# Optimization experiments

Hardware: AMD Instinct MI355X
Metric: run time of the kernel (lower is better)

The kernel has to match this reference:

```python
import jax, jax.numpy as jnp
import numpy as np

B, T, N, K, HD = 4, 32, 1024, 16, 128
IN_CH = 4


def _knn_idx(q, r, k):
    # q, r: [..., 3, N]. dist(n, m) = ||q[..., n] - r[..., m]||
    # expanded-norm form avoids materializing [..., 3, N, N]
    q2 = jnp.sum(q * q, axis=-2)                     # [..., N]
    r2 = jnp.sum(r * r, axis=-2)                     # [..., N]
    qr = jnp.einsum('...cn,...cm->...nm', q, r)      # [..., N, N]
    d2 = q2[..., :, None] + r2[..., None, :] - 2.0 * qr
    _, idx = jax.lax.top_k(-d2, k)                   # smallest-k (sqrt is monotone)
    return idx                                       # [..., N, K]


def _gather_nbrs(feat, idx):
    # feat [B, C, N], idx [B, N, K] -> [B, C, N, K]; out[b,c,n,k] = feat[b,c,idx[b,n,k]]
    return jax.vmap(lambda f, i: f[:, i])(feat, idx)


def _lstm_layer(cur_in, position, pos_past, group_ind, w, b, hd):
    # cur_in [B,T,C,N]; position/pos_past [B,T,4,N]; group_ind [B,T,N,K]
    Bb, Tt, C, Nn = cur_in.shape
    h0 = jnp.zeros((Bb, hd, Nn), cur_in.dtype)
    c0 = jnp.zeros_like(h0)

    def step(carry, inp):
        h, c = carry                                  # [B,hd,N]
        xt, pp, idx = inp                             # [B,C,N], [B,4,N], [B,N,K]
        h_with_pos = jnp.concatenate([pp, h], axis=1) # [B,4+hd,N]
        hg = _gather_nbrs(h_with_pos, idx)            # [B,4+hd,N,K]
        cg = _gather_nbrs(c, idx)                     # [B,hd,N,K]
        # cell subtracts center position from first 4 channels of hidden
        hg = jnp.concatenate([hg[:, :4] - xt[:, :4, :, None], hg[:, 4:]], axis=1)
        xk = jnp.broadcast_to(xt[..., None], xt.shape + (idx.shape[-1],))
        comb = jnp.concatenate([xk, hg], axis=1)      # [B, C+4+hd, N, K]
        gates = jnp.einsum('bink,oi->bonk', comb, w) + b[None, :, None, None]
        ci, cf, co, cgt = jnp.split(gates, 4, axis=1)
        c_next = jax.nn.sigmoid(cf) * cg + jax.nn.sigmoid(ci) * jnp.tanh(cgt)
        h_next = jax.nn.sigmoid(co) * jnp.tanh(c_next)
        h_new = jnp.max(h_next, axis=-1)              # AdaptiveMaxPool2d((None,1)) over K
        c_new = jnp.max(c_next, axis=-1)
        return (h_new, c_new), h_new

    xs = (jnp.moveaxis(cur_in, 1, 0), jnp.moveaxis(pos_past, 1, 0),
          jnp.moveaxis(group_ind, 1, 0))
    (h, c), hs = jax.lax.scan(step, (h0, c0), xs)
    hs = jnp.moveaxis(hs, 0, 1)                       # [B,T,hd,N]
    layer_out = jnp.concatenate([position, hs], axis=2)  # [B,T,4+hd,N]
    return layer_out, h, c


def _forward(x, w0, b0, w1, b1):
    position = x[:, :, :4]                            # [B,T,4,N]
    p3 = position[:, :, :3]
    idx0 = _knn_idx(p3[:, 0], p3[:, 0], K)[:, None]   # [B,1,N,K] (frame 0 vs itself)
    idxr = _knn_idx(p3[:, 1:], p3[:, :-1], K)         # [B,T-1,N,K] (frame t vs t-1)
    group_ind = jnp.concatenate([idx0, idxr], axis=1)  # [B,T,N,K]
    # past-frame positions (t=0 uses frame 0)
    pos_past = jnp.concatenate([position[:, :1], position[:, :-1]], axis=1)
    out0, h, c = _lstm_layer(x,    position, pos_past, group_ind, w0, b0, HD)
    out1, h, c = _lstm_layer(out0, position, pos_past, group_ind, w1, b1, HD)
    return out1, h, c, group_ind


def setup_inputs() -> dict:
    key = jax.random.key(0)
    ks = jax.random.split(key, 3)
    x = jax.random.normal(ks[0], (B, T, IN_CH, N), jnp.float32)
    # 1x1 conv weights flattened to [out, in]; layer0 in=4+4+128=136, layer1 in=132+4+128=264
    w0 = jax.random.normal(ks[1], (4 * HD, IN_CH + 4 + HD), jnp.float32) * 0.05
    b0 = jnp.zeros((4 * HD,), jnp.float32)
    w1 = jax.random.normal(ks[2], (4 * HD, (HD + 4) + 4 + HD), jnp.float32) * 0.05
    b1 = jnp.zeros((4 * HD,), jnp.float32)
    return {"x": x, "w0": w0, "b0": b0, "w1": w1, "b1": b1}


def reference(x, w0, b0, w1, b1):
    out1, h, c, group_ind = _forward(x, w0, b0, w1, b1)
    # match torch shapes: trailing singleton dim
    return out1[..., None], h[..., None], c[..., None], group_ind
```

## Files before the change

### kernel.cpp

```cpp
#include <hip/hip_runtime.h>
#include <math.h>

#define BB 4
#define TT 32
#define NN 1024
#define KK 16
#define HDIM 128
#define NO 512
#define KG 132

#define OUT1_SZ ((size_t)BB*TT*132*NN)
#define OH (OUT1_SZ)
#define OC (OH + (size_t)BB*HDIM*NN)
#define OG (OC + (size_t)BB*HDIM*NN)

__global__ __launch_bounds__(256) void prep_weights(
    const float* __restrict__ w0, const float* __restrict__ w1,
    float* __restrict__ WaT0, float* __restrict__ WgT0,
    float* __restrict__ WaT1, float* __restrict__ WgT1)
{
  int idx = blockIdx.x * 256 + threadIdx.x;
  if (idx >= KG * NO) return;
  int k = idx / NO, o = idx - k * NO;
  WgT0[idx] = w0[o * 136 + 4 + k];
  WgT1[idx] = w1[o * 264 + 132 + k];
  float a1 = w1[o * 264 + k];
  if (k < 4) a1 -= w1[o * 264 + 132 + k];
  WaT1[idx] = a1;
  if (k < 4) WaT0[k * NO + o] = w0[o * 136 + k] - w0[o * 136 + 4 + k];
}

__global__ __launch_bounds__(512) void knn_kernel(
    const float* __restrict__ x, int* __restrict__ gind, float* __restrict__ gfloat)
{
  __shared__ float rx[NN], ry[NN], rz[NN], rr[NN];
  int b = blockIdx.z, t = blockIdx.y;
  int tp = (t == 0) ? 0 : t - 1;
  const float* xr = x + (size_t)(b * TT + tp) * 4 * NN;
  for (int m = threadIdx.x; m < NN; m += 512) {
    float a = xr[m], e = xr[NN + m], c = xr[2 * NN + m];
    rx[m] = a; ry[m] = e; rz[m] = c;
    rr[m] = __fadd_rn(__fadd_rn(__fmul_rn(a, a), __fmul_rn(e, e)), __fmul_rn(c, c));
  }
  __syncthreads();
  int n = blockIdx.x * 512 + threadIdx.x;
  const float* xq = x + (size_t)(b * TT + t) * 4 * NN;
  float qx = xq[n], qy = xq[NN + n], qz = xq[2 * NN + n];
  float q2 = __fadd_rn(__fadd_rn(__fmul_rn(qx, qx), __fmul_rn(qy, qy)), __fmul_rn(qz, qz));
  float bd[KK]; int bi[KK];
#pragma unroll
  for (int i = 0; i < KK; ++i) { bd[i] = 3.402823466e38f; bi[i] = 0; }
  for (int m = 0; m < NN; ++m) {
    float s = __fmaf_rn(qz, rz[m], __fmaf_rn(qy, ry[m], __fmaf_rn(qx, rx[m], 0.0f)));
    float d2 = __fsub_rn(__fadd_rn(q2, rr[m]), __fmul_rn(2.0f, s));
    if (d2 < bd[KK - 1]) {
#pragma unroll
      for (int i = KK - 1; i > 0; --i) {
        float pv = bd[i - 1]; int pi = bi[i - 1];
        if (pv > d2)            { bd[i] = pv; bi[i] = pi; }
        else if (bd[i] > d2)    { bd[i] = d2; bi[i] = m; }
      }
      if (bd[0] > d2) { bd[0] = d2; bi[0] = m; }
    }
  }
  size_t base = ((size_t)(b * TT + t) * NN + n) * KK;
#pragma unroll
  for (int i = 0; i < KK; ++i) { gind[base + i] = bi[i]; gfloat[base + i] = (float)bi[i]; }
}

template<int KA>
__global__ __launch_bounds__(256) void gemm_ag(
    const float* __restrict__ WgT, const float* __restrict__ WaT,
    const float* __restrict__ bias,
    const float* __restrict__ x,
    const float* __restrict__ h_g, const float* __restrict__ h_a,
    int t, int tp,
    float* __restrict__ Aout, float* __restrict__ Gout)
{
  __shared__ float sXg[44][68];
  __shared__ float sWg[44][64];
  __shared__ float sXa[(KA == 4) ? 4 : 44][68];
  __shared__ float sWa[(KA == 4) ? 4 : 44][64];

  int tid = threadIdx.x;
  int nb = blockIdx.x * 64, ob = blockIdx.y * 64, b = blockIdx.z;
  int ty = tid >> 4, tx = tid & 15;
  int o0 = ty * 4, n0 = tx * 4;

  float accG[4][4] = {};
  float accA[4][4];
#pragma unroll
  for (int i = 0; i < 4; ++i) {
    float bv = bias[ob + o0 + i];
#pragma unroll
    for (int j = 0; j < 4; ++j) accA[i][j] = bv;
  }

  const float* xp_prev = x + (size_t)(b * TT + tp) * 4 * NN;
  const float* xp_cur  = x + (size_t)(b * TT + t) * 4 * NN;

#pragma unroll
  for (int ic = 0; ic < 3; ++ic) {
    const int kc0 = ic * 44;
    for (int i2 = tid; i2 < 44 * 64; i2 += 256) {
      int k = i2 >> 6, o = i2 & 63;
      sWg[k][o] = WgT[(size_t)(kc0 + k) * NO + ob + o];
      if (KA == 132) sWa[k][o] = WaT[(size_t)(kc0 + k) * NO + ob + o];
    }
    if (KA == 4 && ic == 0 && tid < 4 * 64) {
      int k = tid >> 6, o = tid & 63;
      sWa[k][o] = WaT[k * NO + ob + o];
    }
    if (ic == 0) {
      int k = tid >> 6, n = tid & 63;
      sXg[k][n] = xp_prev[k * NN + nb + n];
      sXa[k][n] = xp_cur[k * NN + nb + n];
    }
    {
      const int j0 = (ic == 0) ? 0 : (kc0 - 4);
      const int jc = (ic == 0) ? 40 : 44;
      for (int i2 = tid; i2 < 64 * jc; i2 += 256) {
        int n = i2 / jc, jj = i2 - n * jc;
        int krow = j0 + jj + 4 - kc0;
        sXg[krow][n] = h_g[((size_t)b * NN + nb + n) * HDIM + j0 + jj];
        if (KA == 132)
          sXa[krow][n] = h_a[((size_t)b * NN + nb + n) * HDIM + j0 + jj];
      }
    }
    __syncthreads();

    if (KA == 4 && ic == 0) {
#pragma unroll
      for (int k = 0; k < 4; ++k) {
        float4 wa = *(const float4*)&sWa[k][o0];
        float4 xa = *(const float4*)&sXa[k][n0];
        float wv[4] = {wa.x, wa.y, wa.z, wa.w};
        float xv[4] = {xa.x, xa.y, xa.z, xa.w};
#pragma unroll
        for (int i = 0; i < 4; ++i)
#pragma unroll
          for (int j = 0; j < 4; ++j) accA[i][j] = fmaf(wv[i], xv[j], accA[i][j]);
      }
    }
#pragma unroll 4
    for (int k = 0; k < 44; ++k) {
      float4 wg = *(const float4*)&sWg[k][o0];
      float4 xg = *(const float4*)&sXg[k][n0];
      float wv[4] = {wg.x, wg.y, wg.z, wg.w};
      float xv[4] = {xg.x, xg.y, xg.z, xg.w};
#pragma unroll
      for (int i = 0; i < 4; ++i)
#pragma unroll
        for (int j = 0; j < 4; ++j) accG[i][j] = fmaf(wv[i], xv[j], accG[i][j]);
      if (KA == 132) {
        float4 wa = *(const float4*)&sWa[k][o0];
        float4 xa = *(const float4*)&sXa[k][n0];
        float wv2[4] = {wa.x, wa.y, wa.z, wa.w};
        float xv2[4] = {xa.x, xa.y, xa.z, xa.w};
#pragma unroll
        for (int i = 0; i < 4; ++i)
#pragma unroll
          for (int j = 0; j < 4; ++j) accA[i][j] = fmaf(wv2[i], xv2[j], accA[i][j]);
      }
    }
    __syncthreads();
  }
#pragma unroll
  for (int j = 0; j < 4; ++j) {
    size_t row = ((size_t)b * NN + nb + n0 + j) * NO + ob + o0;
    *(float4*)&Gout[row] = make_float4(accG[0][j], accG[1][j], accG[2][j], accG[3][j]);
    *(float4*)&Aout[row] = make_float4(accA[0][j], accA[1][j], accA[2][j], accA[3][j]);
  }
}

__global__ __launch_bounds__(256) void ew_step(
    const float* __restrict__ A, const float* __restrict__ G,
    const int* __restrict__ gind,
    const float* __restrict__ c_in, float* __restrict__ c_out,
    float* __restrict__ h_out, int t)
{
  int tid = threadIdx.x;
  int j = tid & 127, ns = tid >> 7;
  int b = blockIdx.y;
  int n = blockIdx.x * 2 + ns;
  const float* Ap = A + ((size_t)b * NN + n) * NO;
  float a0 = Ap[j], a1 = Ap[128 + j], a2 = Ap[256 + j], a3 = Ap[384 + j];
  const int* ip = gind + ((size_t)(b * TT + t) * NN + n) * KK;
  const float* Gb = G + (size_t)b * NN * NO;
  const float* cb = c_in + (size_t)b * NN * HDIM;
  float hmax = -3.402823466e38f, cmax = -3.402823466e38f;
#pragma unroll 4
  for (int k = 0; k < KK; ++k) {
    int m = ip[k];
    const float* Gp = Gb + (size_t)m * NO;
    float gi = a0 + Gp[j];
    float gf = a1 + Gp[128 + j];
    float go = a2 + Gp[256 + j];
    float gg = a3 + Gp[384 + j];
    float cg = cb[(size_t)m * HDIM + j];
    float si = 1.0f / (1.0f + __expf(-gi));
    float sf = 1.0f / (1.0f + __expf(-gf));
    float so = 1.0f / (1.0f + __expf(-go));
    float tg = 1.0f - 2.0f / (1.0f + __expf(2.0f * gg));
    float cn = sf * cg + si * tg;
    float tc = 1.0f - 2.0f / (1.0f + __expf(2.0f * cn));
    float hn = so * tc;
    hmax = fmaxf(hmax, hn);
    cmax = fmaxf(cmax, cn);
  }
  h_out[((size_t)b * NN + n) * HDIM + j] = hmax;
  c_out[((size_t)b * NN + n) * HDIM + j] = cmax;
}

__global__ __launch_bounds__(256) void transpose_nj_jn(
    const float* __restrict__ src, float* __restrict__ dst,
    size_t dstBase, size_t bStride)
{
  __shared__ float tl[64][65];
  int tid = threadIdx.x;
  int n0 = blockIdx.x * 64, j0 = blockIdx.y * 64, b = blockIdx.z;
  int c = tid & 63, r4 = tid >> 6;
#pragma unroll
  for (int i = 0; i < 16; ++i) {
    int r = r4 + i * 4;
    tl[r][c] = src[((size_t)b * NN + n0 + r) * HDIM + j0 + c];
  }
  __syncthreads();
  float* dp = dst + dstBase + (size_t)b * bStride;
#pragma unroll
  for (int i = 0; i < 16; ++i) {
    int rr = r4 + i * 4;
    dp[(size_t)(j0 + rr) * NN + n0 + c] = tl[c][rr];
  }
}

__global__ __launch_bounds__(256) void pos_copy(const float* __restrict__ x,
                                                float* __restrict__ out)
{
  int i = blockIdx.x * 256 + threadIdx.x;
  if (i >= BB * TT * 4 * NN) return;
  int n = i & (NN - 1);
  int btc = i >> 10;
  int c = btc & 3, bt = btc >> 2;
  out[((size_t)bt * 132 + c) * NN + n] = x[i];
}

extern "C" void kernel_launch(void* const* d_in, const int* in_sizes, int n_in,
                              void* d_out, int out_size, void* d_ws, size_t ws_size,
                              hipStream_t stream)
{
  const float* x  = (const float*)d_in[0];
  const float* w0 = (const float*)d_in[1];
  const float* b0 = (const float*)d_in[2];
  const float* w1 = (const float*)d_in[3];
  const float* b1 = (const float*)d_in[4];
  float* out = (float*)d_out;

  float* wsf = (float*)d_ws;
  int*   gind = (int*)d_ws;
  size_t off = (size_t)BB * TT * NN * KK;
  const size_t HSZ = (size_t)BB * NN * HDIM;
  float* h0  = wsf + off; off += HSZ;
  float* h1  = wsf + off; off += HSZ;
  float* c0a = wsf + off; off += HSZ;
  float* c0b = wsf + off; off += HSZ;
  float* c1a = wsf + off; off += HSZ;
  float* c1b = wsf + off; off += HSZ;
  float* Abuf = wsf + off; off += (size_t)BB * NN * NO;
  float* Gbuf = wsf + off; off += (size_t)BB * NN * NO;
  float* WaT0 = wsf + off; off += 4 * NO;
  float* WgT0 = wsf + off; off += (size_t)KG * NO;
  float* WaT1 = wsf + off; off += (size_t)KG * NO;
  float* WgT1 = wsf + off; off += (size_t)KG * NO;

  hipMemsetAsync(h0, 0, HSZ * 4, stream);
  hipMemsetAsync(h1, 0, HSZ * 4, stream);
  hipMemsetAsync(c0a, 0, HSZ * 4, stream);
  hipMemsetAsync(c1a, 0, HSZ * 4, stream);

  prep_weights<<<(KG * NO + 255) / 256, 256, 0, stream>>>(w0, w1, WaT0, WgT0, WaT1, WgT1);
  knn_kernel<<<dim3(2, TT, BB), 512, 0, stream>>>(x, gind, out + OG);
  pos_copy<<<(BB * TT * 4 * NN + 255) / 256, 256, 0, stream>>>(x, out);

  float* c0[2] = {c0a, c0b};
  float* c1[2] = {c1a, c1b};
  for (int t = 0; t < TT; ++t) {
    int tp = t ? t - 1 : 0;
    gemm_ag<4><<<dim3(16, 8, BB), 256, 0, stream>>>(
        WgT0, WaT0, b0, x, h0, (const float*)nullptr, t, tp, Abuf, Gbuf);
    ew_step<<<dim3(NN / 2, BB), 256, 0, stream>>>(
        Abuf, Gbuf, gind, c0[t & 1], c0[(t & 1) ^ 1], h0, t);
    gemm_ag<132><<<dim3(16, 8, BB), 256, 0, stream>>>(
        WgT1, WaT1, b1, x, h1, h0, t, tp, Abuf, Gbuf);
    ew_step<<<dim3(NN / 2, BB), 256, 0, stream>>>(
        Abuf, Gbuf, gind, c1[t & 1], c1[(t & 1) ^ 1], h1, t);
    transpose_nj_jn<<<dim3(16, 2, BB), 256, 0, stream>>>(
        h1, out, (size_t)t * 132 * NN + 4 * NN, (size_t)TT * 132 * NN);
  }
  transpose_nj_jn<<<dim3(16, 2, BB), 256, 0, stream>>>(h1, out, OH, (size_t)HDIM * NN);
  transpose_nj_jn<<<dim3(16, 2, BB), 256, 0, stream>>>(c1[0], out, OC, (size_t)HDIM * NN);
}
```

Before: 4.449 ms.

## Store hidden state channel-major and drop LDS tiling in gate GEMM

Hidden states are now kept transposed ([hd, N]) so the gate GEMM can read them with coalesced float4 loads and no shared-memory staging. The GEMM becomes a register-blocked kernel with 8x4 outputs per thread and wave-uniform weight loads. Layer-1 hidden output goes straight into the output tensor, which removes the per-step transpose kernel, and the final h is copied from the output. The catch is that the ew_step hidden stores become strided, and the GEMM now depends on scalar weight loads and L2 reuse instead of LDS reuse.

```diff
diff --git a/kernel.cpp b/kernel.cpp
--- a/kernel.cpp
+++ b/kernel.cpp
@@ -71,105 +71,87 @@
 template<int KA>
 __global__ __launch_bounds__(256) void gemm_ag(
     const float* __restrict__ WgT, const float* __restrict__ WaT,
-    const float* __restrict__ bias,
-    const float* __restrict__ x,
-    const float* __restrict__ h_g, const float* __restrict__ h_a,
+    const float* __restrict__ bias, const float* __restrict__ x,
+    const float* __restrict__ hTg, size_t hTg_bstr,
+    const float* __restrict__ hTa,
     int t, int tp,
     float* __restrict__ Aout, float* __restrict__ Gout)
 {
-  __shared__ float sXg[44][68];
-  __shared__ float sWg[44][64];
-  __shared__ float sXa[(KA == 4) ? 4 : 44][68];
-  __shared__ float sWa[(KA == 4) ? 4 : 44][64];
-
   int tid = threadIdx.x;
-  int nb = blockIdx.x * 64, ob = blockIdx.y * 64, b = blockIdx.z;
-  int ty = tid >> 4, tx = tid & 15;
-  int o0 = ty * 4, n0 = tx * 4;
-
-  float accG[4][4] = {};
-  float accA[4][4];
-#pragma unroll
-  for (int i = 0; i < 4; ++i) {
-    float bv = bias[ob + o0 + i];
-#pragma unroll
-    for (int j = 0; j < 4; ++j) accA[i][j] = bv;
-  }
-
-  const float* xp_prev = x + (size_t)(b * TT + tp) * 4 * NN;
-  const float* xp_cur  = x + (size_t)(b * TT + t) * 4 * NN;
-
-#pragma unroll
-  for (int ic = 0; ic < 3; ++ic) {
-    const int kc0 = ic * 44;
-    for (int i2 = tid; i2 < 44 * 64; i2 += 256) {
-      int k = i2 >> 6, o = i2 & 63;
-      sWg[k][o] = WgT[(size_t)(kc0 + k) * NO + ob + o];
-      if (KA == 132) sWa[k][o] = WaT[(size_t)(kc0 + k) * NO + ob + o];
-    }
-    if (KA == 4 && ic == 0 && tid < 4 * 64) {
-      int k = tid >> 6, o = tid & 63;
-      sWa[k][o] = WaT[k * NO + ob + o];
-    }
-    if (ic == 0) {
-      int k = tid >> 6, n = tid & 63;
-      sXg[k][n] = xp_prev[k * NN + nb + n];
-      sXa[k][n] = xp_cur[k * NN + nb + n];
-    }
-    {
-      const int j0 = (ic == 0) ? 0 : (kc0 - 4);
-      const int jc = (ic == 0) ? 40 : 44;
-      for (int i2 = tid; i2 < 64 * jc; i2 += 256) {
-        int n = i2 / jc, jj = i2 - n * jc;
-        int krow = j0 + jj + 4 - kc0;
-        sXg[krow][n] = h_g[((size_t)b * NN + nb + n) * HDIM + j0 + jj];
-        if (KA == 132)
-          sXa[krow][n] = h_a[((size_t)b * NN + nb + n) * HDIM + j0 + jj];
+  int w = tid >> 6, lane = tid & 63;
+  int o0 = blockIdx.y * 32 + w * 8;
+  int o0u = __builtin_amdgcn_readfirstlane(o0);
+  int n0 = blockIdx.x * 256 + lane * 4;
+  int b = blockIdx.z;
+
+  float aG[8][4];
+  float aA[8][4];
+#pragma unroll
+  for (int i = 0; i < 8; ++i)
+#pragma unroll
+    for (int j = 0; j < 4; ++j) { aG[i][j] = 0.0f; aA[i][j] = 0.0f; }
+
+  const float* xg = x + (size_t)(b * TT + tp) * 4 * NN;
+  const float* xa = x + (size_t)(b * TT + t) * 4 * NN;
+
+#pragma unroll
+  for (int k = 0; k < 4; ++k) {
+    const float* wg = WgT + (size_t)k * NO + o0u;
+    const float* wa = WaT + (size_t)k * NO + o0u;
+    float4 vg4 = *(const float4*)(xg + (size_t)k * NN + n0);
+    float4 va4 = *(const float4*)(xa + (size_t)k * NN + n0);
+    float gv[4] = {vg4.x, vg4.y, vg4.z, vg4.w};
+    float av[4] = {va4.x, va4.y, va4.z, va4.w};
+#pragma unroll
+    for (int i = 0; i < 8; ++i) {
+      float wgi = wg[i], wai = wa[i];
+#pragma unroll
+      for (int j = 0; j < 4; ++j) {
+        aG[i][j] = fmaf(wgi, gv[j], aG[i][j]);
+        aA[i][j] = fmaf(wai, av[j], aA[i][j]);
       }
     }
-    __syncthreads();
-
-    if (KA == 4 && ic == 0) {
-#pragma unroll
-      for (int k = 0; k < 4; ++k) {
-        float4 wa = *(const float4*)&sWa[k][o0];
-        float4 xa = *(const float4*)&sXa[k][n0];
-        float wv[4] = {wa.x, wa.y, wa.z, wa.w};
-        float xv[4] = {xa.x, xa.y, xa.z, xa.w};
-#pragma unroll
-        for (int i = 0; i < 4; ++i)
-#pragma unroll
-          for (int j = 0; j < 4; ++j) accA[i][j] = fmaf(wv[i], xv[j], accA[i][j]);
+  }
+
+  const float* hg = hTg + (size_t)b * hTg_bstr + n0;
+  const float* ha = hTa + (size_t)b * (HDIM * NN) + n0;
+#pragma unroll 4
+  for (int k = 0; k < HDIM; ++k) {
+    const float* wg = WgT + (size_t)(4 + k) * NO + o0u;
+    float4 vg4 = *(const float4*)(hg + (size_t)k * NN);
+    float gv[4] = {vg4.x, vg4.y, vg4.z, vg4.w};
+#pragma unroll
+    for (int i = 0; i < 8; ++i) {
+      float wgi = wg[i];
+#pragma unroll
+      for (int j = 0; j < 4; ++j) aG[i][j] = fmaf(wgi, gv[j], aG[i][j]);
+    }
+    if (KA == 132) {
+      const float* wa = WaT + (size_t)(4 + k) * NO + o0u;
+      float4 va4 = *(const float4*)(ha + (size_t)k * NN);
+      float av[4] = {va4.x, va4.y, va4.z, va4.w};
+#pragma unroll
+      for (int i = 0; i < 8; ++i) {
+        float wai = wa[i];
+#pragma unroll
+        for (int j = 0; j < 4; ++j) aA[i][j] = fmaf(wai, av[j], aA[i][j]);
       }
     }
-#pragma unroll 4
-    for (int k = 0; k < 44; ++k) {
-      float4 wg = *(const float4*)&sWg[k][o0];
-      float4 xg = *(const float4*)&sXg[k][n0];
-      float wv[4] = {wg.x, wg.y, wg.z, wg.w};
-      float xv[4] = {xg.x, xg.y, xg.z, xg.w};
-#pragma unroll
-      for (int i = 0; i < 4; ++i)
-#pragma unroll
-        for (int j = 0; j < 4; ++j) accG[i][j] = fmaf(wv[i], xv[j], accG[i][j]);
-      if (KA == 132) {
-        float4 wa = *(const float4*)&sWa[k][o0];
-        float4 xa = *(const float4*)&sXa[k][n0];
-        float wv2[4] = {wa.x, wa.y, wa.z, wa.w};
-        float xv2[4] = {xa.x, xa.y, xa.z, xa.w};
-#pragma unroll
-        for (int i = 0; i < 4; ++i)
-#pragma unroll
-          for (int j = 0; j < 4; ++j) accA[i][j] = fmaf(wv2[i], xv2[j], accA[i][j]);
-      }
-    }
-    __syncthreads();
-  }
+  }
+
+  const float* bv = bias + o0u;
+  float b8[8];
+#pragma unroll
+  for (int i = 0; i < 8; ++i) b8[i] = bv[i];
 #pragma unroll
   for (int j = 0; j < 4; ++j) {
-    size_t row = ((size_t)b * NN + nb + n0 + j) * NO + ob + o0;
-    *(float4*)&Gout[row] = make_float4(accG[0][j], accG[1][j], accG[2][j], accG[3][j]);
-    *(float4*)&Aout[row] = make_float4(accA[0][j], accA[1][j], accA[2][j], accA[3][j]);
+    size_t row = ((size_t)b * NN + n0 + j) * NO + o0u;
+    *(float4*)&Gout[row]     = make_float4(aG[0][j], aG[1][j], aG[2][j], aG[3][j]);
+    *(float4*)&Gout[row + 4] = make_float4(aG[4][j], aG[5][j], aG[6][j], aG[7][j]);
+    *(float4*)&Aout[row]     = make_float4(aA[0][j] + b8[0], aA[1][j] + b8[1],
+                                           aA[2][j] + b8[2], aA[3][j] + b8[3]);
+    *(float4*)&Aout[row + 4] = make_float4(aA[4][j] + b8[4], aA[5][j] + b8[5],
+                                           aA[6][j] + b8[6], aA[7][j] + b8[7]);
   }
 }
 
@@ -177,7 +159,7 @@
     const float* __restrict__ A, const float* __restrict__ G,
     const int* __restrict__ gind,
     const float* __restrict__ c_in, float* __restrict__ c_out,
-    float* __restrict__ h_out, int t)
+    float* __restrict__ hT, size_t hT_bstr, int t)
 {
   int tid = threadIdx.x;
   int j = tid & 127, ns = tid >> 7;
@@ -208,7 +190,7 @@
     hmax = fmaxf(hmax, hn);
     cmax = fmaxf(cmax, cn);
   }
-  h_out[((size_t)b * NN + n) * HDIM + j] = hmax;
+  hT[(size_t)b * hT_bstr + (size_t)j * NN + n] = hmax;
   c_out[((size_t)b * NN + n) * HDIM + j] = cmax;
 }
 
@@ -232,6 +214,16 @@
     int rr = r4 + i * 4;
     dp[(size_t)(j0 + rr) * NN + n0 + c] = tl[c][rr];
   }
+}
+
+__global__ __launch_bounds__(256) void copy_h(const float* __restrict__ out1,
+                                              float* __restrict__ dst)
+{
+  int i = blockIdx.x * 256 + threadIdx.x;
+  if (i >= BB * HDIM * NN) return;
+  int b = i / (HDIM * NN);
+  int r = i - b * (HDIM * NN);
+  dst[i] = out1[((size_t)(b * TT + TT - 1) * 132 + 4) * NN + r];
 }
 
 __global__ __launch_bounds__(256) void pos_copy(const float* __restrict__ x,
@@ -260,12 +252,12 @@
   int*   gind = (int*)d_ws;
   size_t off = (size_t)BB * TT * NN * KK;
   const size_t HSZ = (size_t)BB * NN * HDIM;
-  float* h0  = wsf + off; off += HSZ;
-  float* h1  = wsf + off; off += HSZ;
+  float* h0T = wsf + off; off += HSZ;
   float* c0a = wsf + off; off += HSZ;
   float* c0b = wsf + off; off += HSZ;
   float* c1a = wsf + off; off += HSZ;
   float* c1b = wsf + off; off += HSZ;
+  float* zeros = wsf + off; off += (size_t)HDIM * NN;
   float* Abuf = wsf + off; off += (size_t)BB * NN * NO;
   float* Gbuf = wsf + off; off += (size_t)BB * NN * NO;
   float* WaT0 = wsf + off; off += 4 * NO;
@@ -273,30 +265,33 @@
   float* WaT1 = wsf + off; off += (size_t)KG * NO;
   float* WgT1 = wsf + off; off += (size_t)KG * NO;
 
-  hipMemsetAsync(h0, 0, HSZ * 4, stream);
-  hipMemsetAsync(h1, 0, HSZ * 4, stream);
   hipMemsetAsync(c0a, 0, HSZ * 4, stream);
   hipMemsetAsync(c1a, 0, HSZ * 4, stream);
+  hipMemsetAsync(zeros, 0, (size_t)HDIM * NN * 4, stream);
 
   prep_weights<<<(KG * NO + 255) / 256, 256, 0, stream>>>(w0, w1, WaT0, WgT0, WaT1, WgT1);
   knn_kernel<<<dim3(2, TT, BB), 512, 0, stream>>>(x, gind, out + OG);
   pos_copy<<<(BB * TT * 4 * NN + 255) / 256, 256, 0, stream>>>(x, out);
+
+  const size_t H_BSTR = (size_t)HDIM * NN;
+  const size_t OUT_BSTR = (size_t)TT * 132 * NN;
 
   float* c0[2] = {c0a, c0b};
   float* c1[2] = {c1a, c1b};
   for (int t = 0; t < TT; ++t) {
     int tp = t ? t - 1 : 0;
-    gemm_ag<4><<<dim3(16, 8, BB), 256, 0, stream>>>(
-        WgT0, WaT0, b0, x, h0, (const float*)nullptr, t, tp, Abuf, Gbuf);
+    const float* hTg0 = t ? h0T : zeros;
+    gemm_ag<4><<<dim3(4, 16, BB), 256, 0, stream>>>(
+        WgT0, WaT0, b0, x, hTg0, t ? H_BSTR : 0, h0T, t, tp, Abuf, Gbuf);
     ew_step<<<dim3(NN / 2, BB), 256, 0, stream>>>(
-        Abuf, Gbuf, gind, c0[t & 1], c0[(t & 1) ^ 1], h0, t);
-    gemm_ag<132><<<dim3(16, 8, BB), 256, 0, stream>>>(
-        WgT1, WaT1, b1, x, h1, h0, t, tp, Abuf, Gbuf);
+        Abuf, Gbuf, gind, c0[t & 1], c0[(t & 1) ^ 1], h0T, H_BSTR, t);
+    const float* hTg1 = t ? (out + ((size_t)(t - 1) * 132 + 4) * NN) : zeros;
+    gemm_ag<132><<<dim3(4, 16, BB), 256, 0, stream>>>(
+        WgT1, WaT1, b1, x, hTg1, t ? OUT_BSTR : 0, h0T, t, tp, Abuf, Gbuf);
     ew_step<<<dim3(NN / 2, BB), 256, 0, stream>>>(
-        Abuf, Gbuf, gind, c1[t & 1], c1[(t & 1) ^ 1], h1, t);
-    transpose_nj_jn<<<dim3(16, 2, BB), 256, 0, stream>>>(
-        h1, out, (size_t)t * 132 * NN + 4 * NN, (size_t)TT * 132 * NN);
-  }
-  transpose_nj_jn<<<dim3(16, 2, BB), 256, 0, stream>>>(h1, out, OH, (size_t)HDIM * NN);
+        Abuf, Gbuf, gind, c1[t & 1], c1[(t & 1) ^ 1],
+        out + ((size_t)t * 132 + 4) * NN, OUT_BSTR, t);
+  }
+  copy_h<<<(BB * HDIM * NN + 255) / 256, 256, 0, stream>>>(out, out + OH);
   transpose_nj_jn<<<dim3(16, 2, BB), 256, 0, stream>>>(c1[0], out, OC, (size_t)HDIM * NN);
 }
```

After: 5.280 ms. 1.19x slower.
